# Kernel optimization log

Measured on AMD Instinct MI355X. Metric: run time of the kernel, lower is better.

## Reference

```python
import jax, jax.numpy as jnp
import numpy as np

NUM_HEADS = 4
GROUPS = 8
EPS = 1e-5

def setup_inputs() -> dict:
    key = jax.random.key(0)
    ks = jax.random.split(key, 4)
    C = 256
    x = jax.random.normal(ks[0], (4, C, 64, 64), dtype=jnp.float32)
    qkv_w = jax.random.normal(ks[1], (3 * C, C), dtype=jnp.float32) * (C ** -0.5)
    qkv_b = jnp.zeros((3 * C,), dtype=jnp.float32)
    proj_w = jax.random.normal(ks[2], (C, C), dtype=jnp.float32) * (C ** -0.5)
    proj_b = jnp.zeros((C,), dtype=jnp.float32)
    gamma = jnp.ones((C,), dtype=jnp.float32)
    beta = jnp.zeros((C,), dtype=jnp.float32)
    return {"x": x, "qkv_w": qkv_w, "qkv_b": qkv_b, "proj_w": proj_w, "proj_b": proj_b, "gamma": gamma, "beta": beta}

def group_norm(x, gamma, beta):
    B, C, H, W = x.shape
    xg = x.reshape(B, GROUPS, C // GROUPS, H, W)
    mean = xg.mean(axis=(2, 3, 4), keepdims=True)
    var = xg.var(axis=(2, 3, 4), keepdims=True)
    xn = (xg - mean) * jax.lax.rsqrt(var + EPS)
    xn = xn.reshape(B, C, H, W)
    return xn * gamma[None, :, None, None] + beta[None, :, None, None]

def reference(x, qkv_w, qkv_b, proj_w, proj_b, gamma, beta):
    B, C, H, W = x.shape
    L = H * W
    hd = C // NUM_HEADS
    xn = group_norm(x, gamma, beta)  # (B,C,H,W)
    xf = xn.reshape(B, C, L)  # tokens along last axis
    # 1x1 conv == per-pixel linear: (3C, C) @ (B, C, L)
    qkv = jnp.einsum('oc,bcl->bol', qkv_w, xf) + qkv_b[None, :, None]
    q, k, v = jnp.split(qkv, 3, axis=1)  # each (B,C,L)
    q = q.reshape(B, NUM_HEADS, hd, L)
    k = k.reshape(B, NUM_HEADS, hd, L)
    v = v.reshape(B, NUM_HEADS, hd, L)
    scale = hd ** -0.5
    attn = jnp.einsum('bhdq,bhdk->bhqk', q, k) * scale
    attn = jax.nn.softmax(attn, axis=-1)
    out = jnp.einsum('bhqk,bhdk->bhdq', attn, v)  # (B,h,hd,L)
    out = out.reshape(B, C, L)
    out = jnp.einsum('oc,bcl->bol', proj_w, out) + proj_b[None, :, None]
    return out.reshape(B, C, H, W) + xn
```

## Files before the change

kernel.cpp:

```cpp
#include <hip/hip_runtime.h>
#include <math.h>

#define L 4096
#define LOG2E_O8 0.18033688011112042f

typedef float f32x16 __attribute__((ext_vector_type(16)));
typedef __bf16 bf16x8 __attribute__((ext_vector_type(8)));

static __device__ __forceinline__ float fast_exp2(float x) {
    return __builtin_amdgcn_exp2f(x);
}
static __device__ __forceinline__ unsigned short f2bfu(float f) {
    unsigned int u = __builtin_bit_cast(unsigned int, f);
    u += 0x7fffu + ((u >> 16) & 1u);
    return (unsigned short)(u >> 16);
}
static __device__ __forceinline__ unsigned int cvtpk(float a, float b) {
    unsigned int r;
    asm("v_cvt_pk_bf16_f32 %0, %1, %2" : "=v"(r) : "v"(a), "v"(b));
    return r;
}
static __device__ __forceinline__ void pl32swap(unsigned int& a, unsigned int& b) {
    auto r = __builtin_amdgcn_permlane32_swap(a, b, false, false);
    a = r[0];
    b = r[1];
}
static __device__ __forceinline__ bf16x8 ld_frag_g(const unsigned short* p) {
    uint4 v = *(const uint4*)p;
    return __builtin_bit_cast(bf16x8, v);
}
static __device__ __forceinline__ bf16x8 ld_frag_s(const unsigned short* p) {
    uint4 v = *(const uint4*)p;
    return __builtin_bit_cast(bf16x8, v);
}

__global__ __launch_bounds__(256) void gn_stats_part_kernel(const float* __restrict__ x,
                                                            float2* __restrict__ part) {
    const int blk = blockIdx.x;
    const float4* p = (const float4*)(x + (size_t)blk * 8192);
    float sum = 0.f, sq = 0.f;
    for (int i = threadIdx.x; i < 2048; i += 256) {
        float4 v = p[i];
        sum += (v.x + v.y) + (v.z + v.w);
        sq  += (v.x * v.x + v.y * v.y) + (v.z * v.z + v.w * v.w);
    }
#pragma unroll
    for (int off = 1; off < 64; off <<= 1) {
        sum += __shfl_xor(sum, off);
        sq  += __shfl_xor(sq, off);
    }
    __shared__ float red[8];
    const int t = threadIdx.x;
    if ((t & 63) == 0) { red[(t >> 6) * 2] = sum; red[(t >> 6) * 2 + 1] = sq; }
    __syncthreads();
    if (t == 0) {
        float s = red[0] + red[2] + red[4] + red[6];
        float q = red[1] + red[3] + red[5] + red[7];
        part[blk] = make_float2(s, q);
    }
}

__global__ __launch_bounds__(64) void gn_stats_final_kernel(const float2* __restrict__ part,
                                                            float2* __restrict__ stats) {
    const int bg = threadIdx.x;
    if (bg < 32) {
        float s = 0.f, q = 0.f;
#pragma unroll
        for (int i = 0; i < 16; ++i) {
            float2 v = part[bg * 16 + i];
            s += v.x; q += v.y;
        }
        const float inv_n = 1.0f / (32.0f * L);
        float mean = s * inv_n;
        float var = q * inv_n - mean * mean;
        stats[bg] = make_float2(mean, rsqrtf(var + 1e-5f));
    }
}

__global__ __launch_bounds__(256) void wcvt_kernel(const float* __restrict__ qkv_w,
                                                   const float* __restrict__ proj_w,
                                                   unsigned short* __restrict__ Wqb,
                                                   unsigned short* __restrict__ Wpb) {
    const int i4 = (blockIdx.x * 256 + threadIdx.x) * 4;
    const float* src;
    unsigned short* dst;
    if (i4 < 196608) { src = qkv_w + i4; dst = Wqb + i4; }
    else             { src = proj_w + (i4 - 196608); dst = Wpb + (i4 - 196608); }
    float4 v = *(const float4*)src;
    ushort4 o;
    o.x = f2bfu(v.x); o.y = f2bfu(v.y); o.z = f2bfu(v.z); o.w = f2bfu(v.w);
    *(ushort4*)dst = o;
}

__global__ __launch_bounds__(256) void gn_apply_kernel(const float* __restrict__ x,
                                                       const float* __restrict__ gamma,
                                                       const float* __restrict__ beta,
                                                       const float2* __restrict__ stats,
                                                       unsigned short* __restrict__ xnT) {
    __shared__ float tile[64][68];
    const int t = threadIdx.x;
    const int b = blockIdx.z, c0 = blockIdx.y * 64, l0 = blockIdx.x * 64;
    const int lc = (t & 15) * 4, cr = t >> 4;
#pragma unroll
    for (int p = 0; p < 4; ++p) {
        const int c = c0 + cr + p * 16;
        const float2 st = stats[b * 8 + (c >> 5)];
        const float g = gamma[c] * st.y;
        const float be = beta[c] - st.x * g;
        float4 v = *(const float4*)&x[((size_t)b * 256 + c) * L + l0 + lc];
        float4 o;
        o.x = v.x * g + be; o.y = v.y * g + be; o.z = v.z * g + be; o.w = v.w * g + be;
        *(float4*)&tile[cr + p * 16][lc] = o;
    }
    __syncthreads();
    const int lr = t >> 2, cc = (t & 3) * 16;
    unsigned short* dst = &xnT[((size_t)b * L + l0 + lr) * 256 + c0 + cc];
#pragma unroll
    for (int g4 = 0; g4 < 4; ++g4) {
        ushort4 o4;
        o4.x = f2bfu(tile[cc + g4 * 4 + 0][lr]);
        o4.y = f2bfu(tile[cc + g4 * 4 + 1][lr]);
        o4.z = f2bfu(tile[cc + g4 * 4 + 2][lr]);
        o4.w = f2bfu(tile[cc + g4 * 4 + 3][lr]);
        *(ushort4*)&dst[g4 * 4] = o4;
    }
}

__global__ __launch_bounds__(256) void qkv_gemm_kernel(
        const unsigned short* __restrict__ xnT,
        const unsigned short* __restrict__ Wq,
        const float* __restrict__ bias,
        unsigned short* __restrict__ Qb,
        unsigned short* __restrict__ Kb,
        unsigned short* __restrict__ Vb) {
    const int t = threadIdx.x, lane = t & 63, w = t >> 6;
    const int l5 = lane >> 5, l31 = lane & 31;
    const int wn = w & 1, wm = w >> 1;
    const int n0 = blockIdx.x * 128 + wn * 64;
    const int m0 = blockIdx.y * 128 + wm * 64;
    const int b = blockIdx.z;
    const unsigned short* ap = xnT + ((size_t)b * L + n0 + l31) * 256 + l5 * 8;
    const unsigned short* bp = Wq + (size_t)(m0 + l31) * 256 + l5 * 8;
    f32x16 acc[2][2];
#pragma unroll
    for (int i = 0; i < 2; ++i)
#pragma unroll
        for (int j = 0; j < 2; ++j)
#pragma unroll
            for (int r = 0; r < 16; ++r) acc[i][j][r] = 0.f;
#pragma unroll
    for (int k0 = 0; k0 < 256; k0 += 16) {
        bf16x8 a0 = ld_frag_g(ap + k0);
        bf16x8 a1 = ld_frag_g(ap + 32 * 256 + k0);
        bf16x8 b0 = ld_frag_g(bp + k0);
        bf16x8 b1 = ld_frag_g(bp + 32 * 256 + k0);
        acc[0][0] = __builtin_amdgcn_mfma_f32_32x32x16_bf16(a0, b0, acc[0][0], 0, 0, 0);
        acc[0][1] = __builtin_amdgcn_mfma_f32_32x32x16_bf16(a0, b1, acc[0][1], 0, 0, 0);
        acc[1][0] = __builtin_amdgcn_mfma_f32_32x32x16_bf16(a1, b0, acc[1][0], 0, 0, 0);
        acc[1][1] = __builtin_amdgcn_mfma_f32_32x32x16_bf16(a1, b1, acc[1][1], 0, 0, 0);
    }
    const int sec = m0 >> 8;
    const size_t bh = (size_t)(b * 4 + ((m0 >> 6) & 3));
#pragma unroll
    for (int j = 0; j < 2; ++j) {
        const int m = m0 + j * 32 + l31;
        const int d = m & 63;
        const float bi = bias[m];
        if (sec < 2) {
            unsigned short* dst = (sec ? Kb : Qb) + bh * L * 64 + d;
            const float sc = (sec == 0) ? LOG2E_O8 : 1.0f;
#pragma unroll
            for (int i = 0; i < 2; ++i)
#pragma unroll
                for (int r = 0; r < 16; ++r) {
                    const int n = n0 + i * 32 + (r & 3) + 8 * (r >> 2) + 4 * l5;
                    dst[(size_t)n * 64] = f2bfu((acc[i][j][r] + bi) * sc);
                }
        } else {
            unsigned short* dst = Vb + (bh * 64 + d) * L;
#pragma unroll
            for (int i = 0; i < 2; ++i)
#pragma unroll
                for (int g = 0; g < 4; ++g) {
                    const int n = n0 + i * 32 + 8 * g + 4 * l5;
                    ushort4 st;
                    st.x = f2bfu(acc[i][j][4 * g + 0] + bi);
                    st.y = f2bfu(acc[i][j][4 * g + 1] + bi);
                    st.z = f2bfu(acc[i][j][4 * g + 2] + bi);
                    st.w = f2bfu(acc[i][j][4 * g + 3] + bi);
                    *(ushort4*)&dst[n] = st;
                }
        }
    }
}

__global__ __launch_bounds__(256, 4) void attn_kernel(
        const unsigned short* __restrict__ Qb,
        const unsigned short* __restrict__ Kb,
        const unsigned short* __restrict__ Vb,
        float* __restrict__ Po,
        float* __restrict__ Pl) {
    const int t = threadIdx.x;
    const int lane = t & 63, w = t >> 6;
    const int l5 = lane >> 5, l31 = lane & 31;
    const int n = blockIdx.x;
    const int bh_i = n & 15;
    const int r = n >> 4;
    const int qt = r & 31;
    const int kh = r >> 5;
    const int q0 = qt * 128 + w * 32;
    const size_t bh = (size_t)bh_i;

    __shared__ alignas(16) unsigned short Kt[2][32][72];
    __shared__ alignas(16) unsigned short Vt[2][64][40];

    const unsigned short* qp = Qb + (bh * L + q0 + l31) * 64 + l5 * 8;
    bf16x8 qf[4];
#pragma unroll
    for (int dc = 0; dc < 4; ++dc) qf[dc] = ld_frag_g(qp + dc * 16);

    const int kr = t >> 3, kq = t & 7;
    const int vd = t >> 2, vp = t & 3;
    const unsigned short* kgsrc = Kb + bh * L * 64 + (size_t)kh * 2048 * 64 + kr * 64 + kq * 8;
    const unsigned short* vgsrc = Vb + (bh * 64 + vd) * L + kh * 2048 + vp * 8;

    f32x16 o0, o1;
#pragma unroll
    for (int r2 = 0; r2 < 16; ++r2) { o0[r2] = 0.f; o1[r2] = 0.f; }
    float4 ls = make_float4(0.f, 0.f, 0.f, 0.f);

    {
        uint4 kv = *(const uint4*)kgsrc;
        uint4 vv = *(const uint4*)vgsrc;
        *(uint4*)&Kt[0][kr][kq * 8] = kv;
        *(uint4*)&Vt[0][vd][vp * 8] = vv;
    }
    __syncthreads();

    for (int kc = 0; kc < 64; ++kc) {
        const int buf = kc & 1;
        uint4 knx, vnx;
        if (kc < 63) {
            knx = *(const uint4*)(kgsrc + (size_t)(kc + 1) * 2048);
            vnx = *(const uint4*)(vgsrc + (kc + 1) * 32);
        }
        bf16x8 kf[4], vf[2][2];
#pragma unroll
        for (int dc = 0; dc < 4; ++dc)
            kf[dc] = ld_frag_s(&Kt[buf][l31][dc * 16 + l5 * 8]);
#pragma unroll
        for (int dh = 0; dh < 2; ++dh)
#pragma unroll
            for (int h16 = 0; h16 < 2; ++h16)
                vf[dh][h16] = ld_frag_s(&Vt[buf][dh * 32 + l31][h16 * 16 + l5 * 8]);
        f32x16 s;
#pragma unroll
        for (int r2 = 0; r2 < 16; ++r2) s[r2] = 0.f;
#pragma unroll
        for (int dc = 0; dc < 4; ++dc)
            s = __builtin_amdgcn_mfma_f32_32x32x16_bf16(kf[dc], qf[dc], s, 0, 0, 0);
#pragma unroll
        for (int r2 = 0; r2 < 16; ++r2) s[r2] = fast_exp2(s[r2]);
#pragma unroll
        for (int g = 0; g < 4; ++g) {
            ls.x += s[4 * g + 0];
            ls.y += s[4 * g + 1];
            ls.z += s[4 * g + 2];
            ls.w += s[4 * g + 3];
        }
        unsigned int w0 = cvtpk(s[0],  s[1]);
        unsigned int w1 = cvtpk(s[2],  s[3]);
        unsigned int w2 = cvtpk(s[4],  s[5]);
        unsigned int w3 = cvtpk(s[6],  s[7]);
        unsigned int w4 = cvtpk(s[8],  s[9]);
        unsigned int w5 = cvtpk(s[10], s[11]);
        unsigned int w6 = cvtpk(s[12], s[13]);
        unsigned int w7 = cvtpk(s[14], s[15]);
        pl32swap(w0, w2);
        pl32swap(w1, w3);
        pl32swap(w4, w6);
        pl32swap(w5, w7);
        int4 p0v, p1v;
        p0v.x = (int)w0; p0v.y = (int)w1; p0v.z = (int)w2; p0v.w = (int)w3;
        p1v.x = (int)w4; p1v.y = (int)w5; p1v.z = (int)w6; p1v.w = (int)w7;
        bf16x8 pb0 = __builtin_bit_cast(bf16x8, p0v);
        bf16x8 pb1 = __builtin_bit_cast(bf16x8, p1v);
        o0 = __builtin_amdgcn_mfma_f32_32x32x16_bf16(vf[0][0], pb0, o0, 0, 0, 0);
        o0 = __builtin_amdgcn_mfma_f32_32x32x16_bf16(vf[0][1], pb1, o0, 0, 0, 0);
        o1 = __builtin_amdgcn_mfma_f32_32x32x16_bf16(vf[1][0], pb0, o1, 0, 0, 0);
        o1 = __builtin_amdgcn_mfma_f32_32x32x16_bf16(vf[1][1], pb1, o1, 0, 0, 0);
        if (kc < 63) {
            *(uint4*)&Kt[buf ^ 1][kr][kq * 8] = knx;
            *(uint4*)&Vt[buf ^ 1][vd][vp * 8] = vnx;
        }
        __syncthreads();
    }
    float lrun = (ls.x + ls.y) + (ls.z + ls.w);
    lrun += __shfl_xor(lrun, 32);
    float* pp = Po + ((size_t)(kh * 16 + bh_i) * 4096 + q0 + l31) * 64 + 4 * l5;
#pragma unroll
    for (int g = 0; g < 4; ++g) {
        *(float4*)&pp[8 * g] =
            make_float4(o0[4 * g + 0], o0[4 * g + 1], o0[4 * g + 2], o0[4 * g + 3]);
        *(float4*)&pp[32 + 8 * g] =
            make_float4(o1[4 * g + 0], o1[4 * g + 1], o1[4 * g + 2], o1[4 * g + 3]);
    }
    if (l5 == 0) Pl[(size_t)(kh * 16 + bh_i) * 4096 + q0 + l31] = lrun;
}

__global__ __launch_bounds__(256) void attn_merge_kernel(
        const float* __restrict__ Po,
        const float* __restrict__ Pl,
        unsigned short* __restrict__ aoT) {
    const int t = threadIdx.x;
    const int ri = blockIdx.x * 64 + (t >> 2);
    const int d0 = (t & 3) * 16;
    const int bh = ri >> 12, q = ri & 4095;
    const int b = bh >> 2, h = bh & 3;
    const float l0 = Pl[ri], l1 = Pl[65536 + ri];
    const float inv = 1.f / (l0 + l1);
    const float* p0 = Po + (size_t)ri * 64 + d0;
    const float* p1 = p0 + (size_t)65536 * 64;
    unsigned short* op = aoT + ((size_t)b * L + q) * 256 + h * 64 + d0;
#pragma unroll
    for (int g = 0; g < 2; ++g) {
        float4 a0 = *(const float4*)&p0[g * 8 + 0];
        float4 a1 = *(const float4*)&p0[g * 8 + 4];
        float4 c0 = *(const float4*)&p1[g * 8 + 0];
        float4 c1 = *(const float4*)&p1[g * 8 + 4];
        uint4 st;
        st.x = cvtpk((a0.x + c0.x) * inv, (a0.y + c0.y) * inv);
        st.y = cvtpk((a0.z + c0.z) * inv, (a0.w + c0.w) * inv);
        st.z = cvtpk((a1.x + c1.x) * inv, (a1.y + c1.y) * inv);
        st.w = cvtpk((a1.z + c1.z) * inv, (a1.w + c1.w) * inv);
        *(uint4*)&op[g * 8] = st;
    }
}

__global__ __launch_bounds__(256) void proj_gemm_kernel(
        const unsigned short* __restrict__ aoT,
        const unsigned short* __restrict__ Wp,
        const float* __restrict__ bias,
        const float* __restrict__ x,
        const float* __restrict__ gamma,
        const float* __restrict__ beta,
        const float2* __restrict__ stats,
        float* __restrict__ out) {
    const int t = threadIdx.x, lane = t & 63, w = t >> 6;
    const int l5 = lane >> 5, l31 = lane & 31;
    const int wn = w & 1, wm = w >> 1;
    const int n0 = blockIdx.x * 64 + wn * 32;
    const int m0 = blockIdx.y * 128 + wm * 64;
    const int b = blockIdx.z;
    const unsigned short* ap = aoT + ((size_t)b * L + n0 + l31) * 256 + l5 * 8;
    const unsigned short* bp = Wp + (size_t)(m0 + l31) * 256 + l5 * 8;
    f32x16 acc[2];
#pragma unroll
    for (int j = 0; j < 2; ++j)
#pragma unroll
        for (int r = 0; r < 16; ++r) acc[j][r] = 0.f;
#pragma unroll
    for (int k0 = 0; k0 < 256; k0 += 16) {
        bf16x8 a  = ld_frag_g(ap + k0);
        bf16x8 b0 = ld_frag_g(bp + k0);
        bf16x8 b1 = ld_frag_g(bp + 32 * 256 + k0);
        acc[0] = __builtin_amdgcn_mfma_f32_32x32x16_bf16(a, b0, acc[0], 0, 0, 0);
        acc[1] = __builtin_amdgcn_mfma_f32_32x32x16_bf16(a, b1, acc[1], 0, 0, 0);
    }
#pragma unroll
    for (int j = 0; j < 2; ++j) {
        const int co = m0 + j * 32 + l31;
        const float2 st = stats[b * 8 + (co >> 5)];
        const float g = gamma[co] * st.y;
        const float be = beta[co] - st.x * g + bias[co];
        const float* xr = &x[((size_t)b * 256 + co) * L];
        float* orow = &out[((size_t)b * 256 + co) * L];
#pragma unroll
        for (int q = 0; q < 4; ++q) {
            const int n = n0 + 8 * q + 4 * l5;
            float4 xv = *(const float4*)&xr[n];
            float4 ov;
            ov.x = acc[j][4 * q + 0] + (xv.x * g + be);
            ov.y = acc[j][4 * q + 1] + (xv.y * g + be);
            ov.z = acc[j][4 * q + 2] + (xv.z * g + be);
            ov.w = acc[j][4 * q + 3] + (xv.w * g + be);
            *(float4*)&orow[n] = ov;
        }
    }
}

extern "C" void kernel_launch(void* const* d_in, const int* in_sizes, int n_in,
                              void* d_out, int out_size, void* d_ws, size_t ws_size,
                              hipStream_t stream) {
    const float* x      = (const float*)d_in[0];
    const float* qkv_w  = (const float*)d_in[1];
    const float* qkv_b  = (const float*)d_in[2];
    const float* proj_w = (const float*)d_in[3];
    const float* proj_b = (const float*)d_in[4];
    const float* gamma  = (const float*)d_in[5];
    const float* beta   = (const float*)d_in[6];
    float* out = (float*)d_out;

    char* ws = (char*)d_ws;
    float2* stats       = (float2*)ws;
    unsigned short* Wqb = (unsigned short*)(ws + 512);
    unsigned short* Wpb = (unsigned short*)(ws + 512 + 393216);
    unsigned short* xnT = (unsigned short*)(ws + 524800);
    unsigned short* Qb  = (unsigned short*)(ws + 524800 + 8388608);
    unsigned short* Kb  = Qb + (size_t)16 * L * 64;
    unsigned short* Vb  = Kb + (size_t)16 * L * 64;
    unsigned short* aoT = Vb + (size_t)16 * L * 64;
    float* Po           = (float*)(ws + 42467840);
    float* Pl           = (float*)(ws + 42467840 + 33554432);
    float2* spart       = (float2*)(ws + 524800);

    gn_stats_part_kernel<<<dim3(512), dim3(256), 0, stream>>>(x, spart);
    gn_stats_final_kernel<<<dim3(1), dim3(64), 0, stream>>>(spart, stats);
    wcvt_kernel<<<dim3(256), dim3(256), 0, stream>>>(qkv_w, proj_w, Wqb, Wpb);
    gn_apply_kernel<<<dim3(64, 4, 4), dim3(256), 0, stream>>>(x, gamma, beta, stats, xnT);
    qkv_gemm_kernel<<<dim3(32, 6, 4), dim3(256), 0, stream>>>(xnT, Wqb, qkv_b, Qb, Kb, Vb);
    attn_kernel<<<dim3(1024), dim3(256), 0, stream>>>(Qb, Kb, Vb, Po, Pl);
    attn_merge_kernel<<<dim3(1024), dim3(256), 0, stream>>>(Po, Pl, aoT);
    proj_gemm_kernel<<<dim3(64, 2, 4), dim3(256), 0, stream>>>(aoT, Wpb, proj_b, x, gamma, beta, stats, out);
}
```

Baseline: 221.3 us.

## Split attention key range across two wave groups per block with LDS reduction

Doubles the attention block to 512 threads. Two groups of four waves each process half of the block's key range (1024 keys each) over 32 iterations instead of 64, with separate double-buffered K/V tiles in shared memory. Partial outputs and row sums from the second group are combined through reused LDS before the global write. This shortens the serial key loop per wave and raises wave-level parallelism. The costs are more shared memory, a higher register-pressure target from launch_bounds(512,8), and an extra reduction step.

```diff
diff --git a/kernel.cpp b/kernel.cpp
--- a/kernel.cpp
+++ b/kernel.cpp
@@ -194,7 +194,7 @@
     }
 }
 
-__global__ __launch_bounds__(256, 4) void attn_kernel(
+__global__ __launch_bounds__(512, 8) void attn_kernel(
         const unsigned short* __restrict__ Qb,
         const unsigned short* __restrict__ Kb,
         const unsigned short* __restrict__ Vb,
@@ -202,27 +202,32 @@
         float* __restrict__ Pl) {
     const int t = threadIdx.x;
     const int lane = t & 63, w = t >> 6;
+    const int wq = w & 3, wk = w >> 2;
     const int l5 = lane >> 5, l31 = lane & 31;
     const int n = blockIdx.x;
     const int bh_i = n & 15;
     const int r = n >> 4;
     const int qt = r & 31;
     const int kh = r >> 5;
-    const int q0 = qt * 128 + w * 32;
+    const int q0 = qt * 128 + wq * 32;
     const size_t bh = (size_t)bh_i;
 
-    __shared__ alignas(16) unsigned short Kt[2][32][72];
-    __shared__ alignas(16) unsigned short Vt[2][64][40];
+    __shared__ alignas(16) char smem[38912];
+    auto Kt = (unsigned short(*)[2][32][72])smem;
+    auto Vt = (unsigned short(*)[2][64][40])(smem + 18432);
+    auto comb = (float(*)[64][36])smem;
 
     const unsigned short* qp = Qb + (bh * L + q0 + l31) * 64 + l5 * 8;
     bf16x8 qf[4];
 #pragma unroll
     for (int dc = 0; dc < 4; ++dc) qf[dc] = ld_frag_g(qp + dc * 16);
 
-    const int kr = t >> 3, kq = t & 7;
-    const int vd = t >> 2, vp = t & 3;
-    const unsigned short* kgsrc = Kb + bh * L * 64 + (size_t)kh * 2048 * 64 + kr * 64 + kq * 8;
-    const unsigned short* vgsrc = Vb + (bh * 64 + vd) * L + kh * 2048 + vp * 8;
+    const int ts = t & 255;
+    const int kr = ts >> 3, kq = ts & 7;
+    const int vd = ts >> 2, vp = ts & 3;
+    const int kbase = kh * 2048 + wk * 1024;
+    const unsigned short* kgsrc = Kb + bh * L * 64 + (size_t)kbase * 64 + kr * 64 + kq * 8;
+    const unsigned short* vgsrc = Vb + (bh * 64 + vd) * L + kbase + vp * 8;
 
     f32x16 o0, o1;
 #pragma unroll
@@ -232,27 +237,27 @@
     {
         uint4 kv = *(const uint4*)kgsrc;
         uint4 vv = *(const uint4*)vgsrc;
-        *(uint4*)&Kt[0][kr][kq * 8] = kv;
-        *(uint4*)&Vt[0][vd][vp * 8] = vv;
+        *(uint4*)&Kt[wk][0][kr][kq * 8] = kv;
+        *(uint4*)&Vt[wk][0][vd][vp * 8] = vv;
     }
     __syncthreads();
 
-    for (int kc = 0; kc < 64; ++kc) {
+    for (int kc = 0; kc < 32; ++kc) {
         const int buf = kc & 1;
         uint4 knx, vnx;
-        if (kc < 63) {
+        if (kc < 31) {
             knx = *(const uint4*)(kgsrc + (size_t)(kc + 1) * 2048);
             vnx = *(const uint4*)(vgsrc + (kc + 1) * 32);
         }
         bf16x8 kf[4], vf[2][2];
 #pragma unroll
         for (int dc = 0; dc < 4; ++dc)
-            kf[dc] = ld_frag_s(&Kt[buf][l31][dc * 16 + l5 * 8]);
+            kf[dc] = ld_frag_s(&Kt[wk][buf][l31][dc * 16 + l5 * 8]);
 #pragma unroll
         for (int dh = 0; dh < 2; ++dh)
 #pragma unroll
             for (int h16 = 0; h16 < 2; ++h16)
-                vf[dh][h16] = ld_frag_s(&Vt[buf][dh * 32 + l31][h16 * 16 + l5 * 8]);
+                vf[dh][h16] = ld_frag_s(&Vt[wk][buf][dh * 32 + l31][h16 * 16 + l5 * 8]);
         f32x16 s;
 #pragma unroll
         for (int r2 = 0; r2 < 16; ++r2) s[r2] = 0.f;
@@ -289,23 +294,42 @@
         o0 = __builtin_amdgcn_mfma_f32_32x32x16_bf16(vf[0][1], pb1, o0, 0, 0, 0);
         o1 = __builtin_amdgcn_mfma_f32_32x32x16_bf16(vf[1][0], pb0, o1, 0, 0, 0);
         o1 = __builtin_amdgcn_mfma_f32_32x32x16_bf16(vf[1][1], pb1, o1, 0, 0, 0);
-        if (kc < 63) {
-            *(uint4*)&Kt[buf ^ 1][kr][kq * 8] = knx;
-            *(uint4*)&Vt[buf ^ 1][vd][vp * 8] = vnx;
+        if (kc < 31) {
+            *(uint4*)&Kt[wk][buf ^ 1][kr][kq * 8] = knx;
+            *(uint4*)&Vt[wk][buf ^ 1][vd][vp * 8] = vnx;
         }
         __syncthreads();
     }
     float lrun = (ls.x + ls.y) + (ls.z + ls.w);
     lrun += __shfl_xor(lrun, 32);
-    float* pp = Po + ((size_t)(kh * 16 + bh_i) * 4096 + q0 + l31) * 64 + 4 * l5;
-#pragma unroll
-    for (int g = 0; g < 4; ++g) {
-        *(float4*)&pp[8 * g] =
-            make_float4(o0[4 * g + 0], o0[4 * g + 1], o0[4 * g + 2], o0[4 * g + 3]);
-        *(float4*)&pp[32 + 8 * g] =
-            make_float4(o1[4 * g + 0], o1[4 * g + 1], o1[4 * g + 2], o1[4 * g + 3]);
-    }
-    if (l5 == 0) Pl[(size_t)(kh * 16 + bh_i) * 4096 + q0 + l31] = lrun;
+
+    if (wk == 1) {
+        float* cb = comb[wq][lane];
+#pragma unroll
+        for (int g = 0; g < 4; ++g) {
+            *(float4*)&cb[4 * g] =
+                make_float4(o0[4 * g + 0], o0[4 * g + 1], o0[4 * g + 2], o0[4 * g + 3]);
+            *(float4*)&cb[16 + 4 * g] =
+                make_float4(o1[4 * g + 0], o1[4 * g + 1], o1[4 * g + 2], o1[4 * g + 3]);
+        }
+        cb[32] = lrun;
+    }
+    __syncthreads();
+    if (wk == 0) {
+        const float* cb = comb[wq][lane];
+#pragma unroll
+        for (int r2 = 0; r2 < 16; ++r2) { o0[r2] += cb[r2]; o1[r2] += cb[16 + r2]; }
+        lrun += cb[32];
+        float* pp = Po + ((size_t)(kh * 16 + bh_i) * 4096 + q0 + l31) * 64 + 4 * l5;
+#pragma unroll
+        for (int g = 0; g < 4; ++g) {
+            *(float4*)&pp[8 * g] =
+                make_float4(o0[4 * g + 0], o0[4 * g + 1], o0[4 * g + 2], o0[4 * g + 3]);
+            *(float4*)&pp[32 + 8 * g] =
+                make_float4(o1[4 * g + 0], o1[4 * g + 1], o1[4 * g + 2], o1[4 * g + 3]);
+        }
+        if (l5 == 0) Pl[(size_t)(kh * 16 + bh_i) * 4096 + q0 + l31] = lrun;
+    }
 }
 
 __global__ __launch_bounds__(256) void attn_merge_kernel(
@@ -419,7 +443,7 @@
     wcvt_kernel<<<dim3(256), dim3(256), 0, stream>>>(qkv_w, proj_w, Wqb, Wpb);
     gn_apply_kernel<<<dim3(64, 4, 4), dim3(256), 0, stream>>>(x, gamma, beta, stats, xnT);
     qkv_gemm_kernel<<<dim3(32, 6, 4), dim3(256), 0, stream>>>(xnT, Wqb, qkv_b, Qb, Kb, Vb);
-    attn_kernel<<<dim3(1024), dim3(256), 0, stream>>>(Qb, Kb, Vb, Po, Pl);
+    attn_kernel<<<dim3(1024), dim3(512), 0, stream>>>(Qb, Kb, Vb, Po, Pl);
     attn_merge_kernel<<<dim3(1024), dim3(256), 0, stream>>>(Po, Pl, aoT);
     proj_gemm_kernel<<<dim3(64, 2, 4), dim3(256), 0, stream>>>(aoT, Wpb, proj_b, x, gamma, beta, stats, out);
 }
```

Result: slower. 660.1 us (+198.3%).
